# Performance work log

Hardware: AMD Instinct MI355X
Metric: run time of the kernel (lower is better)

Reference implementation:

```python
import jax, jax.numpy as jnp
import numpy as np

L, B, IN, D, H, IN2D = 1024, 4, 256, 256, 8, 16
HD = D // H  # 32


def setup_inputs() -> dict:
    key = jax.random.key(0)
    ks = jax.random.split(key, 11)
    std = 0.02
    return {
        "s": jax.random.normal(ks[0], (L, B, IN), jnp.float32),
        "_k": jax.random.normal(ks[1], (L, B, IN), jnp.float32),
        "_v": jax.random.normal(ks[2], (L, B, IN), jnp.float32),
        "p": jax.random.normal(ks[3], (B, L, L, IN2D), jnp.float32),
        "Wq": jax.random.normal(ks[4], (IN, D), jnp.float32) * std,
        "Wk": jax.random.normal(ks[5], (IN, D), jnp.float32) * std,
        "Wv": jax.random.normal(ks[6], (IN, D), jnp.float32) * std,
        "Wo": jax.random.normal(ks[7], (D, IN), jnp.float32) * std,
        "bo": jax.random.normal(ks[8], (IN,), jnp.float32) * std,
        "W2d": jax.random.normal(ks[9], (H, IN2D), jnp.float32) * std,
        "b2d": jax.random.normal(ks[10], (H,), jnp.float32) * std,
    }


def reference(s, _k, _v, p, Wq, Wk, Wv, Wo, bo, W2d, b2d):
    # s: (L, B, IN); p: (B, L, L, IN2D)
    w_t = 1.0 / np.sqrt(D)  # dp_attn_norm == 'd_model'
    q = (s @ Wq).reshape(L, B, H, HD) * w_t
    k = (s @ Wk).reshape(L, B, H, HD)
    v = (s @ Wv).reshape(L, B, H, HD)
    # dot-product affinities: (B, H, L, L)
    scores = jnp.einsum('lbhd,mbhd->bhlm', q, k)
    # pairwise bias: mlp_2d(p) -> (B, L, L, H) -> (B, H, L, L)
    bias = jnp.einsum('bijc,hc->bhij', p, W2d) + b2d[None, :, None, None]
    attn = jax.nn.softmax(scores + bias, axis=-1)
    o = jnp.einsum('bhlm,mbhd->lbhd', attn, v).reshape(L, B, D)
    return (o @ Wo + bo,)
```

## Files before the change

### kernel.cpp

```cpp
#include <hip/hip_runtime.h>


typedef __attribute__((ext_vector_type(8))) short short8;
typedef __attribute__((ext_vector_type(4))) float f32x4;
typedef __attribute__((ext_vector_type(2))) _Float16 half2_t;
typedef unsigned short ushort_t;

#define JS_FIXED 4

__device__ inline unsigned short f2bf(float f) {
  unsigned int u = __float_as_uint(f);
  return (unsigned short)((u + 0x7FFFu + ((u >> 16) & 1u)) >> 16);
}

__global__ __launch_bounds__(256) void prep(
    const float* __restrict__ s, const float* __restrict__ Wq,
    const float* __restrict__ Wk, const float* __restrict__ Wv,
    const float* __restrict__ p, const float* __restrict__ W2d,
    const float* __restrict__ b2d,
    ushort_t* __restrict__ q_bf, ushort_t* __restrict__ k_bf, ushort_t* __restrict__ v_t,
    unsigned int* __restrict__ e16)
{
  __shared__ float s_lds[8][256];
  __shared__ __align__(16) float w2d_s[128];
  __shared__ float b2d_s[8];
  const int t = threadIdx.x;

  if (blockIdx.x < 512) {
    const int b = blockIdx.x >> 7;
    const int l0 = (blockIdx.x & 127) << 3;
    for (int rr = 0; rr < 8; ++rr)
      s_lds[rr][t] = s[((size_t)(((l0 + rr) << 2) + b) << 8) + t];
    __syncthreads();
    float aq[8], ak[8], av[8];
#pragma unroll
    for (int rr = 0; rr < 8; ++rr) { aq[rr] = 0.f; ak[rr] = 0.f; av[rr] = 0.f; }
    for (int k = 0; k < 256; ++k) {
      const float wq = Wq[k * 256 + t];
      const float wk = Wk[k * 256 + t];
      const float wv = Wv[k * 256 + t];
#pragma unroll
      for (int rr = 0; rr < 8; ++rr) {
        const float sv = s_lds[rr][k];
        aq[rr] = fmaf(sv, wq, aq[rr]);
        ak[rr] = fmaf(sv, wk, ak[rr]);
        av[rr] = fmaf(sv, wv, av[rr]);
      }
    }
    const int h = t >> 5, dl = t & 31;
#pragma unroll
    for (int rr = 0; rr < 8; ++rr) {
      const int l = l0 + rr;
      q_bf[(((size_t)(b << 10) + l) << 8) + t] = f2bf(aq[rr] * 0.0625f);
      k_bf[((((size_t)((b << 3) + h) << 10) + l) << 5) + dl] = f2bf(ak[rr]);
    }
    short8 vv;
#pragma unroll
    for (int rr = 0; rr < 8; ++rr) vv[rr] = (short)f2bf(av[rr]);
    *(short8*)&v_t[((((size_t)((b << 3) + h) << 5) + dl) << 10) + l0] = vv;
  } else {
    if (t < 128) w2d_s[t] = W2d[t];
    if (t < 8) b2d_s[t] = b2d[t];
    __syncthreads();
    const size_t n = (((size_t)blockIdx.x - 512) << 8) + t;
    const int b = (int)(n >> 20);
    const unsigned int ij = (unsigned int)(n & 0xFFFFFu);
    const float4* p4 = (const float4*)(p + (n << 4));
    const float4 a = p4[0], bb = p4[1], c = p4[2], d = p4[3];
    const float4* w4 = (const float4*)w2d_s;
    float acc[8];
#pragma unroll
    for (int h = 0; h < 8; ++h) {
      const float4 w0 = w4[h * 4 + 0], w1 = w4[h * 4 + 1];
      const float4 w2 = w4[h * 4 + 2], w3 = w4[h * 4 + 3];
      float av = b2d_s[h];
      av += a.x * w0.x + a.y * w0.y + a.z * w0.z + a.w * w0.w;
      av += bb.x * w1.x + bb.y * w1.y + bb.z * w1.z + bb.w * w1.w;
      av += c.x * w2.x + c.y * w2.y + c.z * w2.z + c.w * w2.w;
      av += d.x * w3.x + d.y * w3.y + d.z * w3.z + d.w * w3.w;
      acc[h] = av;
    }
#pragma unroll
    for (int w = 0; w < 4; ++w) {
      half2_t hv;
      hv[0] = (_Float16)acc[2 * w];
      hv[1] = (_Float16)acc[2 * w + 1];
      e16[(((size_t)((b << 2) + w)) << 20) + ij] = __builtin_bit_cast(unsigned int, hv);
    }
  }
}

template <int JS>
__global__ __launch_bounds__(256, 4) void attn_mfma(
    const ushort_t* __restrict__ q_bf, const ushort_t* __restrict__ k_bf,
    const ushort_t* __restrict__ v_t, const unsigned int* __restrict__ ep,
    float* __restrict__ o_part, float* __restrict__ lsum_part)
{
  __shared__ __align__(16) ushort_t p_lds[2][8][16][40];

  const int t = threadIdx.x;
  const int flat = blockIdx.x + (blockIdx.y << 6) + (blockIdx.z << 8);
  const int swz = ((flat & 7) << 7) + (flat >> 3);
  const int i0 = (swz & 63) << 4;
  const int b  = (swz >> 6) & 3;
  const int js = swz >> 8;

  const int w = t >> 6;
  const int l = t & 63;
  const int lrow = l & 15;
  const int lgrp = l >> 4;

  short8 qa[2];
#pragma unroll
  for (int h2 = 0; h2 < 2; ++h2) {
    const int h = (w << 1) + h2;
    qa[h2] = *(const short8*)&q_bf[(((size_t)(b << 10) + i0 + lrow) << 8) + (h << 5) + (lgrp << 3)];
  }

  f32x4 o_acc[2][2];
  float ls[2][4];
#pragma unroll
  for (int h2 = 0; h2 < 2; ++h2) {
#pragma unroll
    for (int nh = 0; nh < 2; ++nh) o_acc[h2][nh] = (f32x4){0.f, 0.f, 0.f, 0.f};
#pragma unroll
    for (int r = 0; r < 4; ++r) ls[h2][r] = 0.f;
  }

  const size_t A0 = (((size_t)((b << 2) + w)) << 20) + ((size_t)(i0 + (lgrp << 2)) << 10) + lrow;

  auto LOADE = [&](int j0, unsigned int (&ub)[2][4]) {
#pragma unroll
    for (int jh = 0; jh < 2; ++jh)
#pragma unroll
      for (int r = 0; r < 4; ++r)
        ub[jh][r] = ep[A0 + ((size_t)r << 10) + (jh << 4) + j0];
  };

  auto COMPUTE = [&](int j0, unsigned int (&ub)[2][4], int pb) {
#pragma unroll
    for (int jh = 0; jh < 2; ++jh) {
#pragma unroll
      for (int h2 = 0; h2 < 2; ++h2) {
        const int h = (w << 1) + h2;
        const short8 kb = *(const short8*)&k_bf[((((size_t)((b << 3) + h) << 10) + j0 + (jh << 4) + lrow) << 5) + (lgrp << 3)];
        f32x4 cc;
#pragma unroll
        for (int r = 0; r < 4; ++r) {
          const half2_t hv = __builtin_bit_cast(half2_t, ub[jh][r]);
          cc[r] = (float)hv[h2];
        }
        f32x4 d = __builtin_amdgcn_mfma_f32_16x16x32_bf16(qa[h2], kb, cc, 0, 0, 0);
#pragma unroll
        for (int r = 0; r < 4; ++r) {
          const float ex = __expf(d[r]);
          ls[h2][r] += ex;
          p_lds[pb][h][(lgrp << 2) + r][(jh << 4) + lrow] = f2bf(ex);
        }
      }
    }
#pragma unroll
    for (int h2 = 0; h2 < 2; ++h2) {
      const int h = (w << 1) + h2;
      const short8 pa = *(const short8*)&p_lds[pb][h][lrow][lgrp << 3];
#pragma unroll
      for (int nh = 0; nh < 2; ++nh) {
        const short8 vb = *(const short8*)&v_t[((((size_t)((b << 3) + h) << 5) + (nh << 4) + lrow) << 10) + j0 + (lgrp << 3)];
        o_acc[h2][nh] = __builtin_amdgcn_mfma_f32_16x16x32_bf16(pa, vb, o_acc[h2][nh], 0, 0, 0);
      }
    }
  };

  constexpr int CHUNK = 1024 / JS;
  constexpr int NT = CHUNK / 32;
  const int jbeg = js * CHUNK;
  const int jlast = jbeg + CHUNK - 32;

  unsigned int ubA[2][4], ubB[2][4];
  LOADE(jbeg, ubA);
#pragma unroll 1
  for (int t2 = 0; t2 < NT; t2 += 2) {
    const int j0 = jbeg + (t2 << 5);
    const int jn1 = (j0 + 32 < jlast) ? (j0 + 32) : jlast;
    const int jn2 = (j0 + 64 < jlast) ? (j0 + 64) : jlast;
    LOADE(jn1, ubB);
    COMPUTE(j0, ubA, 0);
    LOADE(jn2, ubA);
    COMPUTE(j0 + 32, ubB, 1);
  }

#pragma unroll
  for (int h2 = 0; h2 < 2; ++h2) {
#pragma unroll
    for (int r = 0; r < 4; ++r) {
      float v = ls[h2][r];
      v += __shfl_xor(v, 1, 16);
      v += __shfl_xor(v, 2, 16);
      v += __shfl_xor(v, 4, 16);
      v += __shfl_xor(v, 8, 16);
      ls[h2][r] = v;
    }
  }
  const size_t obase = ((size_t)js << 20) + (((size_t)(b << 10) + i0) << 8);
#pragma unroll
  for (int h2 = 0; h2 < 2; ++h2) {
    const int h = (w << 1) + h2;
#pragma unroll
    for (int nh = 0; nh < 2; ++nh) {
      const int d = (h << 5) + (nh << 4) + lrow;
#pragma unroll
      for (int r = 0; r < 4; ++r)
        o_part[obase + ((size_t)((lgrp << 2) + r) << 8) + d] = o_acc[h2][nh][r];
    }
  }
  if (lrow == 0) {
#pragma unroll
    for (int h2 = 0; h2 < 2; ++h2) {
      const int h = (w << 1) + h2;
      float* lp = lsum_part + (((size_t)((js << 5) + (b << 3) + h)) << 10) + i0;
#pragma unroll
      for (int r = 0; r < 4; ++r)
        lp[(lgrp << 2) + r] = ls[h2][r];
    }
  }
}

__global__ __launch_bounds__(256) void out_proj(
    const float* __restrict__ o_part, const float* __restrict__ lsum_part,
    const float* __restrict__ Wo, const float* __restrict__ bo,
    float* __restrict__ out)
{
  constexpr int JS = JS_FIXED;
  __shared__ float o_lds[8][256];
  const int t = threadIdx.x;
  const int r0 = blockIdx.x << 3;
  const int h = t >> 5;
  for (int rr = 0; rr < 8; ++rr) {
    const int r = r0 + rr;
    const int l = r >> 2, bb = r & 3;
    const size_t base = (((size_t)(bb << 10) + l) << 8) + t;
    float acc = 0.f;
#pragma unroll
    for (int js = 0; js < JS; ++js)
      acc += o_part[((size_t)js << 20) + base];
    float lsv = 0.f;
#pragma unroll
    for (int js = 0; js < JS; ++js)
      lsv += lsum_part[(((size_t)((js << 5) + (bb << 3) + h)) << 10) + l];
    o_lds[rr][t] = acc / lsv;
  }
  __syncthreads();
  float accs[8];
#pragma unroll
  for (int rr = 0; rr < 8; ++rr) accs[rr] = 0.f;
  for (int k = 0; k < 256; ++k) {
    const float wo = Wo[k * 256 + t];
#pragma unroll
    for (int rr = 0; rr < 8; ++rr)
      accs[rr] = fmaf(o_lds[rr][k], wo, accs[rr]);
  }
  const float bov = bo[t];
#pragma unroll
  for (int rr = 0; rr < 8; ++rr)
    out[(size_t)(r0 + rr) * 256 + t] = accs[rr] + bov;
}

extern "C" void kernel_launch(void* const* d_in, const int* in_sizes, int n_in,
                              void* d_out, int out_size, void* d_ws, size_t ws_size,
                              hipStream_t stream)
{
  const float* s   = (const float*)d_in[0];
  const float* p   = (const float*)d_in[3];
  const float* Wq  = (const float*)d_in[4];
  const float* Wk  = (const float*)d_in[5];
  const float* Wv  = (const float*)d_in[6];
  const float* Wo  = (const float*)d_in[7];
  const float* bo  = (const float*)d_in[8];
  const float* W2d = (const float*)d_in[9];
  const float* b2d = (const float*)d_in[10];
  float* out = (float*)d_out;

  ushort_t* q_bf = (ushort_t*)d_ws;
  ushort_t* k_bf = q_bf + (1 << 20);
  ushort_t* v_t  = k_bf + (1 << 20);
  unsigned int* e16 = (unsigned int*)(v_t + (1 << 20));
  float* o_part = (float*)((char*)e16 + ((size_t)1 << 26));
  float* lsum_part = o_part + ((size_t)JS_FIXED << 20);

  prep<<<dim3(512 + 16384), dim3(256), 0, stream>>>(s, Wq, Wk, Wv, p, W2d, b2d,
                                                    q_bf, k_bf, v_t, e16);
  attn_mfma<JS_FIXED><<<dim3(64, 4, JS_FIXED), dim3(256), 0, stream>>>(
      q_bf, k_bf, v_t, e16, o_part, lsum_part);
  out_proj<<<dim3(512), dim3(256), 0, stream>>>(o_part, lsum_part, Wo, bo, out);
}
```

Before: 142.7 us.

## Prefetch K/V tiles into registers two steps ahead and single-buffer LDS

K and V fragments are now loaded into registers together with the bias, one tile ahead of use in a double-buffered register scheme, so global load latency is hidden behind the MFMA and exp work. The P staging buffer in LDS shrinks to a single buffer. s_setprio raises wave priority during compute, and launch bounds drop to 3 waves per SIMD to make room for the extra registers. The risks are lower occupancy and a possible LDS read/write hazard: with one P buffer, a wave could overwrite P for the next tile before its own reads of the previous tile complete. Per-wave ownership of heads may make this safe.

```diff
diff --git a/kernel.cpp b/kernel.cpp
--- a/kernel.cpp
+++ b/kernel.cpp
@@ -91,12 +91,12 @@
 }
 
 template <int JS>
-__global__ __launch_bounds__(256, 4) void attn_mfma(
+__global__ __launch_bounds__(256, 3) void attn_mfma(
     const ushort_t* __restrict__ q_bf, const ushort_t* __restrict__ k_bf,
     const ushort_t* __restrict__ v_t, const unsigned int* __restrict__ ep,
     float* __restrict__ o_part, float* __restrict__ lsum_part)
 {
-  __shared__ __align__(16) ushort_t p_lds[2][8][16][40];
+  __shared__ __align__(16) ushort_t p_lds[8][16][40];
 
   const int t = threadIdx.x;
   const int flat = blockIdx.x + (blockIdx.y << 6) + (blockIdx.z << 8);
@@ -129,6 +129,24 @@
 
   const size_t A0 = (((size_t)((b << 2) + w)) << 20) + ((size_t)(i0 + (lgrp << 2)) << 10) + lrow;
 
+  auto LOADK = [&](int j0, short8 (&kb)[2][2]) {
+#pragma unroll
+    for (int h2 = 0; h2 < 2; ++h2) {
+      const int h = (w << 1) + h2;
+#pragma unroll
+      for (int jh = 0; jh < 2; ++jh)
+        kb[h2][jh] = *(const short8*)&k_bf[((((size_t)((b << 3) + h) << 10) + j0 + (jh << 4) + lrow) << 5) + (lgrp << 3)];
+    }
+  };
+  auto LOADV = [&](int j0, short8 (&vb)[2][2]) {
+#pragma unroll
+    for (int h2 = 0; h2 < 2; ++h2) {
+      const int h = (w << 1) + h2;
+#pragma unroll
+      for (int nh = 0; nh < 2; ++nh)
+        vb[h2][nh] = *(const short8*)&v_t[((((size_t)((b << 3) + h) << 5) + (nh << 4) + lrow) << 10) + j0 + (lgrp << 3)];
+    }
+  };
   auto LOADE = [&](int j0, unsigned int (&ub)[2][4]) {
 #pragma unroll
     for (int jh = 0; jh < 2; ++jh)
@@ -137,38 +155,37 @@
         ub[jh][r] = ep[A0 + ((size_t)r << 10) + (jh << 4) + j0];
   };
 
-  auto COMPUTE = [&](int j0, unsigned int (&ub)[2][4], int pb) {
+  auto TILE = [&](short8 (&kb)[2][2], short8 (&vb)[2][2], unsigned int (&ub)[2][4]) {
+    __builtin_amdgcn_s_setprio(1);
 #pragma unroll
     for (int jh = 0; jh < 2; ++jh) {
 #pragma unroll
       for (int h2 = 0; h2 < 2; ++h2) {
         const int h = (w << 1) + h2;
-        const short8 kb = *(const short8*)&k_bf[((((size_t)((b << 3) + h) << 10) + j0 + (jh << 4) + lrow) << 5) + (lgrp << 3)];
         f32x4 cc;
 #pragma unroll
         for (int r = 0; r < 4; ++r) {
           const half2_t hv = __builtin_bit_cast(half2_t, ub[jh][r]);
           cc[r] = (float)hv[h2];
         }
-        f32x4 d = __builtin_amdgcn_mfma_f32_16x16x32_bf16(qa[h2], kb, cc, 0, 0, 0);
+        f32x4 d = __builtin_amdgcn_mfma_f32_16x16x32_bf16(qa[h2], kb[h2][jh], cc, 0, 0, 0);
 #pragma unroll
         for (int r = 0; r < 4; ++r) {
           const float ex = __expf(d[r]);
           ls[h2][r] += ex;
-          p_lds[pb][h][(lgrp << 2) + r][(jh << 4) + lrow] = f2bf(ex);
+          p_lds[h][(lgrp << 2) + r][(jh << 4) + lrow] = f2bf(ex);
         }
       }
     }
 #pragma unroll
     for (int h2 = 0; h2 < 2; ++h2) {
       const int h = (w << 1) + h2;
-      const short8 pa = *(const short8*)&p_lds[pb][h][lrow][lgrp << 3];
-#pragma unroll
-      for (int nh = 0; nh < 2; ++nh) {
-        const short8 vb = *(const short8*)&v_t[((((size_t)((b << 3) + h) << 5) + (nh << 4) + lrow) << 10) + j0 + (lgrp << 3)];
-        o_acc[h2][nh] = __builtin_amdgcn_mfma_f32_16x16x32_bf16(pa, vb, o_acc[h2][nh], 0, 0, 0);
-      }
-    }
+      const short8 pa = *(const short8*)&p_lds[h][lrow][lgrp << 3];
+#pragma unroll
+      for (int nh = 0; nh < 2; ++nh)
+        o_acc[h2][nh] = __builtin_amdgcn_mfma_f32_16x16x32_bf16(pa, vb[h2][nh], o_acc[h2][nh], 0, 0, 0);
+    }
+    __builtin_amdgcn_s_setprio(0);
   };
 
   constexpr int CHUNK = 1024 / JS;
@@ -176,17 +193,24 @@
   const int jbeg = js * CHUNK;
   const int jlast = jbeg + CHUNK - 32;
 
+  short8 kbA[2][2], vbA[2][2], kbB[2][2], vbB[2][2];
   unsigned int ubA[2][4], ubB[2][4];
-  LOADE(jbeg, ubA);
+  LOADK(jbeg, kbA); LOADV(jbeg, vbA); LOADE(jbeg, ubA);
+  LOADK(jbeg + 32, kbB); LOADV(jbeg + 32, vbB); LOADE(jbeg + 32, ubB);
+
 #pragma unroll 1
   for (int t2 = 0; t2 < NT; t2 += 2) {
     const int j0 = jbeg + (t2 << 5);
-    const int jn1 = (j0 + 32 < jlast) ? (j0 + 32) : jlast;
-    const int jn2 = (j0 + 64 < jlast) ? (j0 + 64) : jlast;
-    LOADE(jn1, ubB);
-    COMPUTE(j0, ubA, 0);
-    LOADE(jn2, ubA);
-    COMPUTE(j0 + 32, ubB, 1);
+    TILE(kbA, vbA, ubA);
+    {
+      const int jn = (j0 + 64 < jlast) ? (j0 + 64) : jlast;
+      LOADK(jn, kbA); LOADV(jn, vbA); LOADE(jn, ubA);
+    }
+    TILE(kbB, vbB, ubB);
+    {
+      const int jn = (j0 + 96 < jlast) ? (j0 + 96) : jlast;
+      LOADK(jn, kbB); LOADV(jn, vbB); LOADE(jn, ubB);
+    }
   }
 
 #pragma unroll
```

Result: no change. 143.9 us (+0.9%).
